# Performance work log

Hardware: AMD Instinct MI355X
Metric: run time of the kernel (lower is better)

## Reference

```python
import jax, jax.numpy as jnp
import numpy as np

B, S, NX, NH = 2, 2048, 1024, 16
HD = NX // NH  # head dim = 64

def setup_inputs() -> dict:
    key = jax.random.key(0)
    k1, k2, k3 = jax.random.split(key, 3)
    return {
        "x": jax.random.normal(k1, (B, S, NX), dtype=jnp.float32),
        "c_attn_w": jax.random.normal(k2, (NX, 3 * NX), dtype=jnp.float32) * 0.02,
        "c_attn_b": jnp.zeros((3 * NX,), dtype=jnp.float32),
        "c_proj_w": jax.random.normal(k3, (NX, NX), dtype=jnp.float32) * 0.02,
        "c_proj_b": jnp.zeros((NX,), dtype=jnp.float32),
    }

def reference(x, c_attn_w, c_attn_b, c_proj_w, c_proj_b):
    b, s, nx = x.shape
    # fused QKV projection (Conv1D == affine on last dim)
    qkv = x @ c_attn_w + c_attn_b                      # [b, s, 3*nx]
    q, k, v = jnp.split(qkv, 3, axis=-1)
    # split heads -> [b, h, s, d]
    q = q.reshape(b, s, NH, HD).transpose(0, 2, 1, 3)
    k = k.reshape(b, s, NH, HD).transpose(0, 2, 1, 3)
    v = v.reshape(b, s, NH, HD).transpose(0, 2, 1, 3)
    # scaled scores with causal mask (masked_fill -1e10, matching original)
    w = jnp.einsum("bhqd,bhkd->bhqk", q, k) / jnp.sqrt(jnp.float32(HD))
    causal = jnp.tril(jnp.ones((s, s), dtype=bool))    # [s, s]
    w = jnp.where(causal[None, None, :, :], w, jnp.float32(-1e10))
    w = jax.nn.softmax(w, axis=-1)
    a = jnp.einsum("bhqk,bhkd->bhqd", w, v)            # [b, h, s, d]
    # merge heads
    a = a.transpose(0, 2, 1, 3).reshape(b, s, nx)
    # output projection (dropout is identity in eval)
    return a @ c_proj_w + c_proj_b
```

## Files before the change

### kernel.cpp

```cpp
#include <hip/hip_runtime.h>
#include <cstdint>

typedef unsigned short u16;
typedef unsigned int u32;
typedef float f32x4 __attribute__((ext_vector_type(4)));
typedef __bf16 bf16x8 __attribute__((ext_vector_type(8)));
typedef __bf16 bf16x4 __attribute__((ext_vector_type(4)));
typedef u16 u16x8 __attribute__((ext_vector_type(8)));

#define B_ 2
#define S_ 2048
#define NX_ 1024
#define NH_ 16
#define HD_ 64
#define T3_ 3072
#define M_ 4096
#define SCL 0.18033688011112042f

__device__ __forceinline__ u16 bfbits(float f) {
    __bf16 h = (__bf16)f;
    return __builtin_bit_cast(u16, h);
}

__device__ __forceinline__ void gload_lds16(const void* g, void* l) {
    auto gp = reinterpret_cast<const __attribute__((address_space(1))) u32*>(
        reinterpret_cast<uintptr_t>(g));
    auto lp = reinterpret_cast<__attribute__((address_space(3))) u32*>(
        reinterpret_cast<uintptr_t>(l));
    __builtin_amdgcn_global_load_lds(gp, lp, 16, 0, 0);
}

__global__ __launch_bounds__(256) void prep_kernel(const float* __restrict__ x,
                                                   u16* __restrict__ xb,
                                                   const float* __restrict__ w1,
                                                   u16* __restrict__ w1t,
                                                   const float* __restrict__ w2,
                                                   u16* __restrict__ w2t) {
    __shared__ float tile[32][33];
    int bid = blockIdx.x;
    if (bid < 4096) {
        int i = (bid * 256 + threadIdx.x) * 4;
        float4 v = *reinterpret_cast<const float4*>(x + i);
        bf16x4 o;
        o[0] = (__bf16)v.x; o[1] = (__bf16)v.y; o[2] = (__bf16)v.z; o[3] = (__bf16)v.w;
        *reinterpret_cast<bf16x4*>(xb + i) = o;
        return;
    }
    const float* W; u16* WT; int N, lb;
    if (bid < 4096 + 3072) { W = w1; WT = w1t; N = T3_; lb = bid - 4096; }
    else                   { W = w2; WT = w2t; N = NX_; lb = bid - 7168; }
    const int K = NX_;
    int nbx = N >> 5;
    int nb = (lb % nbx) << 5;
    int kb = (lb / nbx) << 5;
    int tx = threadIdx.x & 31, ty = threadIdx.x >> 5;
#pragma unroll
    for (int i = 0; i < 32; i += 8)
        tile[ty + i][tx] = W[(size_t)(kb + ty + i) * N + nb + tx];
    __syncthreads();
#pragma unroll
    for (int i = 0; i < 32; i += 8)
        WT[(size_t)(nb + ty + i) * K + kb + tx] = bfbits(tile[tx][ty + i]);
}

#define BM 128
#define BN 128
#define BK 64
__global__ __launch_bounds__(256) void gemm_bt_kernel(const u16* __restrict__ A,
                                                      const u16* __restrict__ Bt,
                                                      const float* __restrict__ bias,
                                                      u16* __restrict__ Cb,
                                                      float* __restrict__ Cf,
                                                      u16* __restrict__ Vt,
                                                      int vcol0, int qcols,
                                                      int M, int N, int K) {
    __shared__ u16 a_lds[2][BM * BK];
    __shared__ u16 b_lds[2][BN * BK];
    int nbn = N / BN;
    int nwg = gridDim.x;
    int orig = blockIdx.x;
    int wg = (orig & 7) * (nwg >> 3) + (orig >> 3);
    int bm = wg / nbn, bn = wg % nbn;
    int t = threadIdx.x;
    int w = t >> 6, l = t & 63, lg = l >> 4, lr = l & 15;
    int wr = w >> 1, wc = w & 1;
    const u16* Abase = A + (size_t)bm * BM * K;
    const u16* Bbase = Bt + (size_t)bn * BN * K;

    f32x4 zero4 = {0.f, 0.f, 0.f, 0.f};
    f32x4 acc[4][4];
#pragma unroll
    for (int m = 0; m < 4; ++m)
#pragma unroll
        for (int n = 0; n < 4; ++n) acc[m][n] = zero4;

    auto stage = [&](int kt, int bs) {
#pragma unroll
        for (int it = 0; it < 4; ++it) {
            int idx = it * 256 + t;
            int row = idx >> 3, ck = idx & 7;
            int cds = ck ^ (row & 7);
            int ubase = (it * 256 + w * 64) * 8;
            gload_lds16(Abase + (size_t)row * K + kt * BK + cds * 8, &a_lds[bs][ubase]);
            gload_lds16(Bbase + (size_t)row * K + kt * BK + cds * 8, &b_lds[bs][ubase]);
        }
    };

    stage(0, 0);
    __syncthreads();

    int nkt = K / BK;
    for (int kt = 0; kt < nkt; ++kt) {
        int cur = kt & 1;
        if (kt + 1 < nkt) stage(kt + 1, cur ^ 1);

#pragma unroll
        for (int ks = 0; ks < 2; ++ks) {
            int ck = (ks * 4 + lg) ^ (lr & 7);
            bf16x8 af[4], bf[4];
#pragma unroll
            for (int m = 0; m < 4; ++m)
                af[m] = *reinterpret_cast<const bf16x8*>(
                    &a_lds[cur][(wr * 64 + m * 16 + lr) * BK + ck * 8]);
#pragma unroll
            for (int n = 0; n < 4; ++n)
                bf[n] = *reinterpret_cast<const bf16x8*>(
                    &b_lds[cur][(wc * 64 + n * 16 + lr) * BK + ck * 8]);
            __builtin_amdgcn_s_setprio(1);
#pragma unroll
            for (int m = 0; m < 4; ++m)
#pragma unroll
                for (int n = 0; n < 4; ++n)
                    acc[m][n] = __builtin_amdgcn_mfma_f32_16x16x32_bf16(
                        af[m], bf[n], acc[m][n], 0, 0, 0);
            __builtin_amdgcn_s_setprio(0);
        }
        __syncthreads();
    }

#pragma unroll
    for (int n = 0; n < 4; ++n) {
        int col0 = bn * BN + wc * 64 + n * 16;
        int col = col0 + lr;
        float bv = bias[col];
        float sc = (col0 < qcols) ? SCL : 1.0f;
        bool isv = (Vt != nullptr) && (col0 >= vcol0);
#pragma unroll
        for (int m = 0; m < 4; ++m) {
            int row0 = bm * BM + wr * 64 + m * 16 + lg * 4;
            if (isv) {
                int nv = col - vcol0, hh = nv >> 6, dd = nv & 63;
                int bb = row0 >> 11, ss = row0 & 2047;
                bf16x4 pk;
#pragma unroll
                for (int r = 0; r < 4; ++r) pk[r] = (__bf16)(acc[m][n][r] + bv);
                *reinterpret_cast<bf16x4*>(
                    Vt + (((size_t)(bb * 16 + hh) * 64 + dd) << 11) + ss) = pk;
            } else {
#pragma unroll
                for (int r = 0; r < 4; ++r) {
                    float v = (acc[m][n][r] + bv) * sc;
                    if (Cf) Cf[(size_t)(row0 + r) * N + col] = v;
                    else    Cb[(size_t)(row0 + r) * N + col] = bfbits(v);
                }
            }
        }
    }
}

__global__ __launch_bounds__(512) void attn_kernel(const u16* __restrict__ qkv,
                                                   const u16* __restrict__ Vt,
                                                   u16* __restrict__ outa) {
    __shared__ u16 k_lds[2][4096];
    __shared__ u16 v_lds[2][4096];
    __shared__ u16 p_lds[8192];

    int bid = blockIdx.x;
    int g = bid & 31;
    int j = bid >> 5;
    int qt = (j < 8) ? (15 - j) : (j - 8);
    int b = g >> 4, h = g & 15;
    int t = threadIdx.x, w = t >> 6, l = t & 63, lg = l >> 4, lr = l & 15;
    const u16* base = qkv + (size_t)b * S_ * T3_;
    const u16* vbase = Vt + (size_t)g * 64 * S_;
    int prow = w * 16 + lr;
    int qb = qt * 128;
    int qrow = qb + w * 16 + lr;

    int srow = w * 8 + (l >> 3);
    auto stage = [&](int kt2, int bs) {
        int kb2 = kt2 * 64;
        int ckg = (l & 7) ^ (srow & 7);
        gload_lds16(base + (size_t)(kb2 + srow) * T3_ + NX_ + h * 64 + ckg * 8,
                    &k_lds[bs][w * 512]);
        gload_lds16(vbase + (size_t)srow * S_ + kb2 + ckg * 8,
                    &v_lds[bs][w * 512]);
    };

    f32x4 zero4 = {0.f, 0.f, 0.f, 0.f};

    bf16x8 qf[2];
#pragma unroll
    for (int ks = 0; ks < 2; ++ks)
        qf[ks] = *reinterpret_cast<const bf16x8*>(
            base + (size_t)qrow * T3_ + h * 64 + ks * 32 + lg * 8);

    f32x4 oacc[4];
#pragma unroll
    for (int dc = 0; dc < 4; ++dc) oacc[dc] = zero4;
    float mrun = -1e30f, lrun = 0.f;
    int nkt = 2 * qt + 2;
    int tw = 2 * qt + (w >> 2);

    stage(0, 0);
    __syncthreads();

    for (int kt = 0; kt < nkt; ++kt) {
        int cur = kt & 1;
        if (kt + 1 < nkt) stage(kt + 1, cur ^ 1);

        if (kt <= tw) {
            int kb = kt * 64;
            f32x4 sacc[4];
#pragma unroll
            for (int kn = 0; kn < 4; ++kn) sacc[kn] = zero4;
            __builtin_amdgcn_s_setprio(1);
#pragma unroll
            for (int ks = 0; ks < 2; ++ks) {
#pragma unroll
                for (int kn = 0; kn < 4; ++kn) {
                    bf16x8 kf = *reinterpret_cast<const bf16x8*>(
                        &k_lds[cur][(kn * 16 + lr) * 64 + (((ks * 4 + lg) ^ (lr & 7)) * 8)]);
                    sacc[kn] = __builtin_amdgcn_mfma_f32_16x16x32_bf16(
                        kf, qf[ks], sacc[kn], 0, 0, 0);
                }
            }
            __builtin_amdgcn_s_setprio(0);

            if (kt == tw) {
#pragma unroll
                for (int kn = 0; kn < 4; ++kn)
#pragma unroll
                    for (int r = 0; r < 4; ++r)
                        if (kb + kn * 16 + lg * 4 + r > qrow) sacc[kn][r] = -1e30f;
            }

            float mx = -1e30f;
#pragma unroll
            for (int kn = 0; kn < 4; ++kn) {
                float a0 = fmaxf(sacc[kn][0], sacc[kn][1]);
                float a1 = fmaxf(sacc[kn][2], sacc[kn][3]);
                mx = fmaxf(mx, fmaxf(a0, a1));
            }
            mx = fmaxf(mx, __shfl_xor(mx, 16));
            mx = fmaxf(mx, __shfl_xor(mx, 32));

            bool noresc = __all(mx <= mrun + 1.5f);
            float mnew = noresc ? mrun : fmaxf(mrun, mx);

            float rs = 0.f;
#pragma unroll
            for (int kn = 0; kn < 4; ++kn)
#pragma unroll
                for (int r = 0; r < 4; ++r) {
                    float pv = exp2f(sacc[kn][r] - mnew);
                    sacc[kn][r] = pv;
                    rs += pv;
                }
            rs += __shfl_xor(rs, 16);
            rs += __shfl_xor(rs, 32);

            if (noresc) {
                lrun += rs;
            } else {
                float fsc = exp2f(mrun - mnew);
                mrun = mnew;
                lrun = lrun * fsc + rs;
                float f0 = __shfl(fsc, lg * 4 + 0);
                float f1 = __shfl(fsc, lg * 4 + 1);
                float f2 = __shfl(fsc, lg * 4 + 2);
                float f3 = __shfl(fsc, lg * 4 + 3);
#pragma unroll
                for (int dc = 0; dc < 4; ++dc) {
                    oacc[dc][0] *= f0; oacc[dc][1] *= f1;
                    oacc[dc][2] *= f2; oacc[dc][3] *= f3;
                }
            }

#pragma unroll
            for (int kn = 0; kn < 4; ++kn) {
                bf16x4 pb;
                pb[0] = (__bf16)sacc[kn][0]; pb[1] = (__bf16)sacc[kn][1];
                pb[2] = (__bf16)sacc[kn][2]; pb[3] = (__bf16)sacc[kn][3];
                int byteoff = prow * 128 + (((2 * kn + (lg >> 1)) ^ (prow & 7)) * 16) + (lg & 1) * 8;
                *reinterpret_cast<bf16x4*>(reinterpret_cast<char*>(p_lds) + byteoff) = pb;
            }

            __builtin_amdgcn_s_setprio(1);
#pragma unroll
            for (int ks = 0; ks < 2; ++ks) {
                bf16x8 pf = *reinterpret_cast<const bf16x8*>(
                    reinterpret_cast<char*>(p_lds) + prow * 128 + (((ks * 4 + lg) ^ (prow & 7)) * 16));
#pragma unroll
                for (int dc = 0; dc < 4; ++dc) {
                    bf16x8 vf = *reinterpret_cast<const bf16x8*>(
                        &v_lds[cur][(dc * 16 + lr) * 64 + (((ks * 4 + lg) ^ (lr & 7)) * 8)]);
                    oacc[dc] = __builtin_amdgcn_mfma_f32_16x16x32_bf16(
                        pf, vf, oacc[dc], 0, 0, 0);
                }
            }
            __builtin_amdgcn_s_setprio(0);
        }
        __syncthreads();
    }

    float inv = 1.f / lrun;
    float i0 = __shfl(inv, lg * 4 + 0);
    float i1 = __shfl(inv, lg * 4 + 1);
    float i2 = __shfl(inv, lg * 4 + 2);
    float i3 = __shfl(inv, lg * 4 + 3);
    u16* ob = outa + (size_t)b * S_ * NX_;
#pragma unroll
    for (int r = 0; r < 4; ++r) {
        float ir = (r == 0) ? i0 : (r == 1) ? i1 : (r == 2) ? i2 : i3;
        int row = qb + w * 16 + lg * 4 + r;
#pragma unroll
        for (int dc = 0; dc < 4; ++dc)
            ob[(size_t)row * NX_ + h * 64 + dc * 16 + lr] = bfbits(oacc[dc][r] * ir);
    }
}

extern "C" void kernel_launch(void* const* d_in, const int* in_sizes, int n_in,
                              void* d_out, int out_size, void* d_ws, size_t ws_size,
                              hipStream_t stream) {
    const float* x        = (const float*)d_in[0];
    const float* c_attn_w = (const float*)d_in[1];
    const float* c_attn_b = (const float*)d_in[2];
    const float* c_proj_w = (const float*)d_in[3];
    const float* c_proj_b = (const float*)d_in[4];
    float* out = (float*)d_out;

    u16* xb     = (u16*)d_ws;
    u16* wqkvT  = xb + (size_t)M_ * NX_;
    u16* wprojT = wqkvT + (size_t)T3_ * NX_;
    u16* qkv    = wprojT + (size_t)NX_ * NX_;
    u16* attno  = xb;
    u16* Vtp    = (u16*)d_out;

    prep_kernel<<<8192, 256, 0, stream>>>(x, xb, c_attn_w, wqkvT, c_proj_w, wprojT);
    gemm_bt_kernel<<<(M_ / BM) * (T3_ / BN), 256, 0, stream>>>(
        xb, wqkvT, c_attn_b, qkv, nullptr, Vtp, 2 * NX_, NX_, M_, T3_, NX_);
    attn_kernel<<<512, 512, 0, stream>>>(qkv, Vtp, attno);
    gemm_bt_kernel<<<(M_ / BM) * (NX_ / BN), 256, 0, stream>>>(
        attno, wprojT, c_proj_b, nullptr, out, nullptr, 0, 0, M_, NX_, NX_);
}
```

Measured before the change: 115.1 us.

## Widen attention key tile from 64 to 128 to halve barrier iterations

The attention kernel now stages 128 keys per iteration instead of 64, doubling the K/V LDS buffers and processing eight score fragments per wave before the softmax update and PV accumulation. This halves the number of loop iterations, barriers and softmax reductions per block, while the causal mask is applied only on the diagonal tile. In exchange, LDS use and register pressure rise, and waves whose rows end early now compute over masked keys in the final tile where before they skipped it.

```diff
diff --git a/kernel.cpp b/kernel.cpp
--- a/kernel.cpp
+++ b/kernel.cpp
@@ -171,8 +171,8 @@
 __global__ __launch_bounds__(512) void attn_kernel(const u16* __restrict__ qkv,
                                                    const u16* __restrict__ Vt,
                                                    u16* __restrict__ outa) {
-    __shared__ u16 k_lds[2][4096];
-    __shared__ u16 v_lds[2][4096];
+    __shared__ u16 k_lds[2][8192];
+    __shared__ u16 v_lds[2][8192];
     __shared__ u16 p_lds[8192];
 
     int bid = blockIdx.x;
@@ -187,14 +187,19 @@
     int qb = qt * 128;
     int qrow = qb + w * 16 + lr;
 
-    int srow = w * 8 + (l >> 3);
     auto stage = [&](int kt2, int bs) {
-        int kb2 = kt2 * 64;
-        int ckg = (l & 7) ^ (srow & 7);
-        gload_lds16(base + (size_t)(kb2 + srow) * T3_ + NX_ + h * 64 + ckg * 8,
-                    &k_lds[bs][w * 512]);
-        gload_lds16(vbase + (size_t)srow * S_ + kb2 + ckg * 8,
-                    &v_lds[bs][w * 512]);
+        int kb2 = kt2 * 128;
+#pragma unroll
+        for (int p = 0; p < 2; ++p) {
+            int slot = w * 128 + p * 64 + l;
+            int ubase = (w * 128 + p * 64) * 8;
+            int rowK = slot >> 3, ckK = (slot & 7) ^ (rowK & 7);
+            gload_lds16(base + (size_t)(kb2 + rowK) * T3_ + NX_ + h * 64 + ckK * 8,
+                        &k_lds[bs][ubase]);
+            int rowV = slot >> 4, ckV = (slot & 15) ^ (rowV & 7);
+            gload_lds16(vbase + (size_t)rowV * S_ + kb2 + ckV * 8,
+                        &v_lds[bs][ubase]);
+        }
     };
 
     f32x4 zero4 = {0.f, 0.f, 0.f, 0.f};
@@ -209,8 +214,7 @@
 #pragma unroll
     for (int dc = 0; dc < 4; ++dc) oacc[dc] = zero4;
     float mrun = -1e30f, lrun = 0.f;
-    int nkt = 2 * qt + 2;
-    int tw = 2 * qt + (w >> 2);
+    int nkt = qt + 1;
 
     stage(0, 0);
     __syncthreads();
@@ -219,92 +223,94 @@
         int cur = kt & 1;
         if (kt + 1 < nkt) stage(kt + 1, cur ^ 1);
 
-        if (kt <= tw) {
-            int kb = kt * 64;
-            f32x4 sacc[4];
-#pragma unroll
-            for (int kn = 0; kn < 4; ++kn) sacc[kn] = zero4;
-            __builtin_amdgcn_s_setprio(1);
-#pragma unroll
-            for (int ks = 0; ks < 2; ++ks) {
-#pragma unroll
-                for (int kn = 0; kn < 4; ++kn) {
-                    bf16x8 kf = *reinterpret_cast<const bf16x8*>(
-                        &k_lds[cur][(kn * 16 + lr) * 64 + (((ks * 4 + lg) ^ (lr & 7)) * 8)]);
-                    sacc[kn] = __builtin_amdgcn_mfma_f32_16x16x32_bf16(
-                        kf, qf[ks], sacc[kn], 0, 0, 0);
-                }
-            }
-            __builtin_amdgcn_s_setprio(0);
-
-            if (kt == tw) {
-#pragma unroll
-                for (int kn = 0; kn < 4; ++kn)
-#pragma unroll
-                    for (int r = 0; r < 4; ++r)
-                        if (kb + kn * 16 + lg * 4 + r > qrow) sacc[kn][r] = -1e30f;
-            }
-
-            float mx = -1e30f;
-#pragma unroll
-            for (int kn = 0; kn < 4; ++kn) {
-                float a0 = fmaxf(sacc[kn][0], sacc[kn][1]);
-                float a1 = fmaxf(sacc[kn][2], sacc[kn][3]);
-                mx = fmaxf(mx, fmaxf(a0, a1));
-            }
-            mx = fmaxf(mx, __shfl_xor(mx, 16));
-            mx = fmaxf(mx, __shfl_xor(mx, 32));
-
-            bool noresc = __all(mx <= mrun + 1.5f);
-            float mnew = noresc ? mrun : fmaxf(mrun, mx);
-
-            float rs = 0.f;
-#pragma unroll
-            for (int kn = 0; kn < 4; ++kn)
-#pragma unroll
-                for (int r = 0; r < 4; ++r) {
-                    float pv = exp2f(sacc[kn][r] - mnew);
-                    sacc[kn][r] = pv;
-                    rs += pv;
-                }
-            rs += __shfl_xor(rs, 16);
-            rs += __shfl_xor(rs, 32);
-
-            if (noresc) {
-                lrun += rs;
-            } else {
-                float fsc = exp2f(mrun - mnew);
-                mrun = mnew;
-                lrun = lrun * fsc + rs;
-                float f0 = __shfl(fsc, lg * 4 + 0);
-                float f1 = __shfl(fsc, lg * 4 + 1);
-                float f2 = __shfl(fsc, lg * 4 + 2);
-                float f3 = __shfl(fsc, lg * 4 + 3);
-#pragma unroll
-                for (int dc = 0; dc < 4; ++dc) {
-                    oacc[dc][0] *= f0; oacc[dc][1] *= f1;
-                    oacc[dc][2] *= f2; oacc[dc][3] *= f3;
-                }
-            }
-
-#pragma unroll
-            for (int kn = 0; kn < 4; ++kn) {
+        int kb = kt * 128;
+        f32x4 sacc[8];
+#pragma unroll
+        for (int kn = 0; kn < 8; ++kn) sacc[kn] = zero4;
+        __builtin_amdgcn_s_setprio(1);
+#pragma unroll
+        for (int ks = 0; ks < 2; ++ks) {
+#pragma unroll
+            for (int kn = 0; kn < 8; ++kn) {
+                bf16x8 kf = *reinterpret_cast<const bf16x8*>(
+                    &k_lds[cur][(kn * 16 + lr) * 64 + (((ks * 4 + lg) ^ (lr & 7)) * 8)]);
+                sacc[kn] = __builtin_amdgcn_mfma_f32_16x16x32_bf16(
+                    kf, qf[ks], sacc[kn], 0, 0, 0);
+            }
+        }
+        __builtin_amdgcn_s_setprio(0);
+
+        if (kt == qt) {
+#pragma unroll
+            for (int kn = 0; kn < 8; ++kn)
+#pragma unroll
+                for (int r = 0; r < 4; ++r)
+                    if (kb + kn * 16 + lg * 4 + r > qrow) sacc[kn][r] = -1e30f;
+        }
+
+        float mx = -1e30f;
+#pragma unroll
+        for (int kn = 0; kn < 8; ++kn) {
+            float a0 = fmaxf(sacc[kn][0], sacc[kn][1]);
+            float a1 = fmaxf(sacc[kn][2], sacc[kn][3]);
+            mx = fmaxf(mx, fmaxf(a0, a1));
+        }
+        mx = fmaxf(mx, __shfl_xor(mx, 16));
+        mx = fmaxf(mx, __shfl_xor(mx, 32));
+
+        bool noresc = __all(mx <= mrun + 1.5f);
+        float mnew = noresc ? mrun : fmaxf(mrun, mx);
+
+        float rs = 0.f;
+#pragma unroll
+        for (int kn = 0; kn < 8; ++kn)
+#pragma unroll
+            for (int r = 0; r < 4; ++r) {
+                float pv = exp2f(sacc[kn][r] - mnew);
+                sacc[kn][r] = pv;
+                rs += pv;
+            }
+        rs += __shfl_xor(rs, 16);
+        rs += __shfl_xor(rs, 32);
+
+        if (noresc) {
+            lrun += rs;
+        } else {
+            float fsc = exp2f(mrun - mnew);
+            mrun = mnew;
+            lrun = lrun * fsc + rs;
+            float f0 = __shfl(fsc, lg * 4 + 0);
+            float f1 = __shfl(fsc, lg * 4 + 1);
+            float f2 = __shfl(fsc, lg * 4 + 2);
+            float f3 = __shfl(fsc, lg * 4 + 3);
+#pragma unroll
+            for (int dc = 0; dc < 4; ++dc) {
+                oacc[dc][0] *= f0; oacc[dc][1] *= f1;
+                oacc[dc][2] *= f2; oacc[dc][3] *= f3;
+            }
+        }
+
+#pragma unroll
+        for (int half = 0; half < 2; ++half) {
+#pragma unroll
+            for (int kn2 = 0; kn2 < 4; ++kn2) {
+                int kn = half * 4 + kn2;
                 bf16x4 pb;
                 pb[0] = (__bf16)sacc[kn][0]; pb[1] = (__bf16)sacc[kn][1];
                 pb[2] = (__bf16)sacc[kn][2]; pb[3] = (__bf16)sacc[kn][3];
-                int byteoff = prow * 128 + (((2 * kn + (lg >> 1)) ^ (prow & 7)) * 16) + (lg & 1) * 8;
+                int byteoff = prow * 128 + (((2 * kn2 + (lg >> 1)) ^ (prow & 7)) * 16) + (lg & 1) * 8;
                 *reinterpret_cast<bf16x4*>(reinterpret_cast<char*>(p_lds) + byteoff) = pb;
             }
-
             __builtin_amdgcn_s_setprio(1);
 #pragma unroll
-            for (int ks = 0; ks < 2; ++ks) {
+            for (int ks2 = 0; ks2 < 2; ++ks2) {
                 bf16x8 pf = *reinterpret_cast<const bf16x8*>(
-                    reinterpret_cast<char*>(p_lds) + prow * 128 + (((ks * 4 + lg) ^ (prow & 7)) * 16));
+                    reinterpret_cast<char*>(p_lds) + prow * 128 + (((ks2 * 4 + lg) ^ (prow & 7)) * 16));
 #pragma unroll
                 for (int dc = 0; dc < 4; ++dc) {
                     bf16x8 vf = *reinterpret_cast<const bf16x8*>(
-                        &v_lds[cur][(dc * 16 + lr) * 64 + (((ks * 4 + lg) ^ (lr & 7)) * 8)]);
+                        &v_lds[cur][(dc * 16 + lr) * 128 +
+                                    (((half * 8 + ks2 * 4 + lg) ^ (lr & 7)) * 8)]);
                     oacc[dc] = __builtin_amdgcn_mfma_f32_16x16x32_bf16(
                         pf, vf, oacc[dc], 0, 0, 0);
                 }
```

New measurement: 109.4 us. -5.0%, faster.
